# Kernel tuning notes

Hardware: AMD Instinct MI355X
Metric: run time of the kernel (lower is better)

Reference implementation:

```python
import jax, jax.numpy as jnp
import numpy as np

B, L, D = 2, 2048, 2048
NUM_HEADS = 32
KV_GROUPS = 8
GROUP_SIZE = NUM_HEADS // KV_GROUPS  # 4
HEAD_DIM = D // NUM_HEADS            # 64


def _rope_tables(L, hd):
    # standard RoPE angle tables, duplicated across halves to width hd
    inv_freq = 1.0 / (10000.0 ** (np.arange(0, hd, 2, dtype=np.float32) / hd))
    ang = np.arange(L, dtype=np.float32)[:, None] * inv_freq[None, :]  # [L, hd/2]
    cos = np.concatenate([np.cos(ang), np.cos(ang)], axis=-1)
    sin = np.concatenate([np.sin(ang), np.sin(ang)], axis=-1)
    return jnp.asarray(cos), jnp.asarray(sin)


def setup_inputs() -> dict:
    key = jax.random.key(0)
    ks = jax.random.split(key, 6)
    x = jax.random.normal(ks[0], (B, L, D), dtype=jnp.float32)
    mask = jnp.triu(jnp.ones((L, L), dtype=bool), k=1)  # causal: True above diag
    cos, sin = _rope_tables(L, HEAD_DIM)
    s = 0.02
    Wq = jax.random.normal(ks[1], (D, D), dtype=jnp.float32) * s
    Wk = jax.random.normal(ks[2], (D, KV_GROUPS * HEAD_DIM), dtype=jnp.float32) * s
    Wv = jax.random.normal(ks[3], (D, KV_GROUPS * HEAD_DIM), dtype=jnp.float32) * s
    Wo = jax.random.normal(ks[4], (D, D), dtype=jnp.float32) * s
    bo = jnp.zeros((D,), dtype=jnp.float32)
    return {"x": x, "mask": mask, "cos": cos, "sin": sin,
            "Wq": Wq, "Wk": Wk, "Wv": Wv, "Wo": Wo, "bo": bo}


def _apply_rope(t, cos, sin):
    # t: [B, H, L, hd]
    hd = t.shape[-1]
    t1, t2 = t[..., : hd // 2], t[..., hd // 2:]
    rotated = jnp.concatenate([-t2, t1], axis=-1)
    return t * cos[None, None, :, :] + rotated * sin[None, None, :, :]


def reference(x, mask, cos, sin, Wq, Wk, Wv, Wo, bo):
    Bv, Lv, Dv = x.shape
    hd = HEAD_DIM
    q = (x @ Wq).reshape(Bv, Lv, NUM_HEADS, hd).transpose(0, 2, 1, 3)   # [B,H,L,hd]
    k = (x @ Wk).reshape(Bv, Lv, KV_GROUPS, hd).transpose(0, 2, 1, 3)   # [B,G,L,hd]
    v = (x @ Wv).reshape(Bv, Lv, KV_GROUPS, hd).transpose(0, 2, 1, 3)
    q = _apply_rope(q, cos, sin)
    k = _apply_rope(k, cos, sin)
    k = jnp.repeat(k, GROUP_SIZE, axis=1)  # [B,H,L,hd]
    v = jnp.repeat(v, GROUP_SIZE, axis=1)
    scores = jnp.einsum('bhqd,bhkd->bhqk', q, k) / jnp.sqrt(jnp.float32(hd))
    scores = jnp.where(mask[None, None, :, :], -jnp.inf, scores)
    attn = jax.nn.softmax(scores, axis=-1)
    out = jnp.einsum('bhqk,bhkd->bhqd', attn, v)         # [B,H,L,hd]
    out = out.transpose(0, 2, 1, 3).reshape(Bv, Lv, Dv)  # [B,L,D]
    return out @ Wo + bo
```

## Files before the change

### kernel.cpp

```cpp
#include <hip/hip_runtime.h>
#include <cstdint>

typedef unsigned short UST;
typedef __bf16 v8bf __attribute__((ext_vector_type(8)));
typedef float v4f __attribute__((ext_vector_type(4)));

static __device__ __forceinline__ UST f2b(float f) {
  union { float f; uint32_t u; } c; c.f = f;
  uint32_t u = c.u;
  u += 0x7fffu + ((u >> 16) & 1u);
  return (UST)(u >> 16);
}
static __device__ __forceinline__ float b2f(UST h) {
  union { uint32_t u; float f; } c; c.u = ((uint32_t)h) << 16;
  return c.f;
}
static __device__ __forceinline__ uint32_t cvtpk(float lo, float hi) {
  uint32_t r;
  asm("v_cvt_pk_bf16_f32 %0, %1, %2" : "=v"(r) : "v"(lo), "v"(hi));
  return r;
}
static __device__ __forceinline__ float fexp2(float x) {
  float r;
  asm("v_exp_f32 %0, %1" : "=v"(r) : "v"(x));
  return r;
}

static __device__ __forceinline__ void gl_lds16(const UST* g, UST* l) {
  __builtin_amdgcn_global_load_lds(
      (const __attribute__((address_space(1))) void*)g,
      (__attribute__((address_space(3))) void*)l, 16, 0, 0);
}

__global__ __launch_bounds__(256) void k_cast(const float* __restrict__ src,
                                              UST* __restrict__ dst) {
  size_t i = (size_t)blockIdx.x * 256 + threadIdx.x;
  const float4* s4 = reinterpret_cast<const float4*>(src) + 2 * i;
  float4 a = s4[0], b = s4[1];
  union { UST s[8]; uint4 v; } r;
  r.s[0] = f2b(a.x); r.s[1] = f2b(a.y); r.s[2] = f2b(a.z); r.s[3] = f2b(a.w);
  r.s[4] = f2b(b.x); r.s[5] = f2b(b.y); r.s[6] = f2b(b.z); r.s[7] = f2b(b.w);
  reinterpret_cast<uint4*>(dst)[i] = r.v;
}

__global__ __launch_bounds__(256) void k_castT(const float* __restrict__ W,
                                               UST* __restrict__ dst, int N, int K) {
  __shared__ float tile[32][33];
  int nt = blockIdx.x * 32, kt = blockIdx.y * 32;
  int tx = threadIdx.x, ty = threadIdx.y;
#pragma unroll
  for (int r = 0; r < 4; ++r)
    tile[ty + r * 8][tx] = W[(size_t)(kt + ty + r * 8) * N + nt + tx];
  __syncthreads();
#pragma unroll
  for (int r = 0; r < 4; ++r)
    dst[(size_t)(nt + ty + r * 8) * K + kt + tx] = f2b(tile[tx][ty + r * 8]);
}

template <int EPI>
__global__ __launch_bounds__(256) void k_gemm(const UST* __restrict__ A,
                                              const UST* __restrict__ Bt,
                                              void* __restrict__ Cv,
                                              const float* __restrict__ bias,
                                              int M, int N, int K) {
  __shared__ __align__(16) UST a_s[128 * 32];
  __shared__ __align__(16) UST b_s[128 * 32];
  int tid = threadIdx.x;
  int lane = tid & 63, w = tid >> 6;
  int lr = lane & 15, lg = lane >> 4;
  int wr = w >> 1, wc = w & 1;
  int mBlk = blockIdx.y * 128, nBlk = blockIdx.x * 128;

  v4f acc[4][4];
#pragma unroll
  for (int i = 0; i < 4; ++i)
#pragma unroll
    for (int j = 0; j < 4; ++j) acc[i][j] = (v4f){0.f, 0.f, 0.f, 0.f};

  int stR = tid >> 2, stC = (tid & 3) * 8;
  const UST* Ag = A + (size_t)(mBlk + stR) * K + stC;
  const UST* Bg = Bt + (size_t)(nBlk + stR) * K + stC;
  UST* aL = a_s + w * 512;
  UST* bL = b_s + w * 512;
  size_t radv = (size_t)64 * K;

  for (int k0 = 0; k0 < K; k0 += 32) {
    __syncthreads();
    gl_lds16(Ag, aL);
    gl_lds16(Ag + radv, aL + 2048);
    gl_lds16(Bg, bL);
    gl_lds16(Bg + radv, bL + 2048);
    Ag += 32; Bg += 32;
    __syncthreads();
    v8bf af[4], bfv[4];
#pragma unroll
    for (int mt = 0; mt < 4; ++mt)
      af[mt] = *(const v8bf*)&a_s[(wr * 64 + mt * 16 + lr) * 32 + lg * 8];
#pragma unroll
    for (int nt = 0; nt < 4; ++nt)
      bfv[nt] = *(const v8bf*)&b_s[(wc * 64 + nt * 16 + lr) * 32 + lg * 8];
#pragma unroll
    for (int mt = 0; mt < 4; ++mt)
#pragma unroll
      for (int nt = 0; nt < 4; ++nt)
        acc[mt][nt] = __builtin_amdgcn_mfma_f32_16x16x32_bf16(af[mt], bfv[nt],
                                                              acc[mt][nt], 0, 0, 0);
  }

  int row0 = mBlk + wr * 64 + lg * 4;
  int col0 = nBlk + wc * 64 + lr;
#pragma unroll
  for (int mt = 0; mt < 4; ++mt)
#pragma unroll
    for (int nt = 0; nt < 4; ++nt)
#pragma unroll
      for (int r = 0; r < 4; ++r) {
        int row = row0 + mt * 16 + r;
        int col = col0 + nt * 16;
        if constexpr (EPI == 0) {
          ((UST*)Cv)[(size_t)row * N + col] = f2b(acc[mt][nt][r]);
        } else {
          ((float*)Cv)[(size_t)row * N + col] = acc[mt][nt][r] + bias[col];
        }
      }
}

__global__ __launch_bounds__(256) void k_rope(const UST* __restrict__ qkv,
                                              const float* __restrict__ cosT,
                                              const float* __restrict__ sinT,
                                              UST* __restrict__ qh,
                                              UST* __restrict__ kh) {
  int idx = blockIdx.x * 256 + threadIdx.x;
  int d = idx & 31;
  int hh = (idx >> 5) % 40;
  int row = idx / 1280;
  int l = row & 2047, b = row >> 11;
  int col = (hh < 32) ? hh * 64 : 2048 + (hh - 32) * 64;
  float t1 = b2f(qkv[(size_t)row * 3072 + col + d]);
  float t2 = b2f(qkv[(size_t)row * 3072 + col + d + 32]);
  float c = cosT[l * 64 + d], s = sinT[l * 64 + d];
  float o1 = t1 * c - t2 * s;
  float o2 = t2 * c + t1 * s;
  if (hh < 32) {
    size_t base = (((size_t)b * 32 + hh) * 2048 + l) * 64 + d;
    qh[base] = f2b(o1 * 0.125f);
    qh[base + 32] = f2b(o2 * 0.125f);
  } else {
    size_t base = (((size_t)b * 8 + (hh - 32)) * 2048 + l) * 64 + d;
    kh[base] = f2b(o1);
    kh[base + 32] = f2b(o2);
  }
}

__global__ __launch_bounds__(256) void k_vtrans(const UST* __restrict__ qkv,
                                                UST* __restrict__ vt) {
  __shared__ __align__(16) UST tl[64][72];
  int lt = blockIdx.x, bg = blockIdx.y;
  int b = bg >> 3, g = bg & 7;
  int t = threadIdx.x;
  int li = t >> 2, d0 = (t & 3) * 16;
  const UST* src = qkv + (size_t)(b * 2048 + lt * 64 + li) * 3072 + 2560 + g * 64 + d0;
  *(uint4*)&tl[li][d0] = *(const uint4*)src;
  *(uint4*)&tl[li][d0 + 8] = *(const uint4*)(src + 8);
  __syncthreads();
  int d = t >> 2, l0 = (t & 3) * 16;
  union { UST u[8]; uint4 v; } r0, r1;
#pragma unroll
  for (int e = 0; e < 8; ++e) r0.u[e] = tl[l0 + e][d];
#pragma unroll
  for (int e = 0; e < 8; ++e) r1.u[e] = tl[l0 + 8 + e][d];
  UST* dstp = vt + (size_t)((b * 8 + g) * 64 + d) * 2048 + (size_t)lt * 64 + l0;
  *(uint4*)dstp = r0.v;
  *(uint4*)(dstp + 8) = r1.v;
}

__global__ __launch_bounds__(512, 4) void k_attn(const UST* __restrict__ qh,
                                                 const UST* __restrict__ kh,
                                                 const UST* __restrict__ vt,
                                                 UST* __restrict__ outp) {
  __shared__ __align__(16) UST k_s[128 * 72];
  __shared__ __align__(16) UST v_s[64 * 136];
  __shared__ __align__(16) UST p_s[8][16 * 136];
  int bx = blockIdx.x, h = blockIdx.y, b = blockIdx.z;
  int g = h >> 2;
  int tid = threadIdx.x, w = tid >> 6, lane = tid & 63;
  int lr = lane & 15, lg = lane >> 4;

  int ksr = tid >> 2, ksc = (tid & 3) * 16;
  int vsr = tid >> 3, vsc = (tid & 7) * 16;
  const UST* kbase = kh + ((size_t)(b * 8 + g) * 2048 + ksr) * 64 + ksc;
  const UST* vbase = vt + ((size_t)(b * 8 + g) * 64 + vsr) * 2048 + vsc;
  UST* kdst = &k_s[ksr * 72 + ksc];
  UST* vdst = &v_s[vsr * 136 + vsc];

  for (int half = 0; half < 2; ++half) {
    int qt = half ? (15 - bx) : bx;
    int qbase = qt * 128 + w * 16;

    const UST* qp = qh + ((size_t)(b * 32 + h) * 2048 + qbase + lr) * 64 + lg * 8;
    v8bf qf0 = *(const v8bf*)qp;
    v8bf qf1 = *(const v8bf*)(qp + 32);

    float m = -1e30f, ls = 0.f;
    v4f o[4];
#pragma unroll
    for (int dt = 0; dt < 4; ++dt) o[dt] = (v4f){0.f, 0.f, 0.f, 0.f};

    __syncthreads();
    uint4 pk0 = *(const uint4*)kbase, pk1 = *(const uint4*)(kbase + 8);
    uint4 pv0 = *(const uint4*)vbase, pv1 = *(const uint4*)(vbase + 8);
    *(uint4*)kdst = pk0; *(uint4*)(kdst + 8) = pk1;
    *(uint4*)vdst = pv0; *(uint4*)(vdst + 8) = pv1;

    for (int j = 0; j <= qt; ++j) {
      __syncthreads();
      bool pref = (j < qt);
      if (pref) {
        const UST* kg = kbase + (size_t)(j + 1) * 8192;
        const UST* vg = vbase + (j + 1) * 128;
        pk0 = *(const uint4*)kg; pk1 = *(const uint4*)(kg + 8);
        pv0 = *(const uint4*)vg; pv1 = *(const uint4*)(vg + 8);
      }

      v4f st[8];
#pragma unroll
      for (int kt = 0; kt < 8; ++kt) {
        const UST* kr = &k_s[(kt * 16 + lr) * 72 + lg * 8];
        v8bf kf0 = *(const v8bf*)kr;
        v8bf kf1 = *(const v8bf*)(kr + 32);
        v4f z = (v4f){0.f, 0.f, 0.f, 0.f};
        z = __builtin_amdgcn_mfma_f32_16x16x32_bf16(kf0, qf0, z, 0, 0, 0);
        z = __builtin_amdgcn_mfma_f32_16x16x32_bf16(kf1, qf1, z, 0, 0, 0);
        st[kt] = z;
      }
      if (j == qt) {
        int qg = qbase + lr;
#pragma unroll
        for (int kt = 0; kt < 8; ++kt)
#pragma unroll
          for (int r = 0; r < 4; ++r) {
            int kg2 = j * 128 + kt * 16 + 4 * lg + r;
            if (kg2 > qg) st[kt][r] = -1e30f;
          }
      }

      float t0 = fmaxf(fmaxf(st[0][0], st[0][1]), fmaxf(st[0][2], st[0][3]));
      float t1 = fmaxf(fmaxf(st[1][0], st[1][1]), fmaxf(st[1][2], st[1][3]));
      float t2 = fmaxf(fmaxf(st[2][0], st[2][1]), fmaxf(st[2][2], st[2][3]));
      float t3 = fmaxf(fmaxf(st[3][0], st[3][1]), fmaxf(st[3][2], st[3][3]));
      float t4 = fmaxf(fmaxf(st[4][0], st[4][1]), fmaxf(st[4][2], st[4][3]));
      float t5 = fmaxf(fmaxf(st[5][0], st[5][1]), fmaxf(st[5][2], st[5][3]));
      float t6 = fmaxf(fmaxf(st[6][0], st[6][1]), fmaxf(st[6][2], st[6][3]));
      float t7 = fmaxf(fmaxf(st[7][0], st[7][1]), fmaxf(st[7][2], st[7][3]));
      float mx = fmaxf(fmaxf(fmaxf(t0, t1), fmaxf(t2, t3)),
                       fmaxf(fmaxf(t4, t5), fmaxf(t6, t7)));
      mx = fmaxf(mx, __shfl_xor(mx, 16));
      mx = fmaxf(mx, __shfl_xor(mx, 32));

      if (!__all(mx <= m + 8.f)) {
        float mn = fmaxf(m, mx);
        float al = __expf(m - mn);
        m = mn;
        ls *= al;
#pragma unroll
        for (int r = 0; r < 4; ++r) {
          float ar = __shfl(al, 4 * lg + r);
          o[0][r] *= ar; o[1][r] *= ar; o[2][r] *= ar; o[3][r] *= ar;
        }
      }

      constexpr float LOG2E = 1.44269504f;
      float mlog = m * LOG2E;
      float rs = 0.f;
      UST* pw = &p_s[w][lr * 136 + 4 * lg];
#pragma unroll
      for (int kt = 0; kt < 8; ++kt) {
        float p0 = fexp2(__builtin_fmaf(st[kt][0], LOG2E, -mlog));
        float p1 = fexp2(__builtin_fmaf(st[kt][1], LOG2E, -mlog));
        float p2 = fexp2(__builtin_fmaf(st[kt][2], LOG2E, -mlog));
        float p3 = fexp2(__builtin_fmaf(st[kt][3], LOG2E, -mlog));
        rs += (p0 + p1) + (p2 + p3);
        uint2 q2;
        q2.x = cvtpk(p0, p1);
        q2.y = cvtpk(p2, p3);
        *(uint2*)(pw + kt * 16) = q2;
      }
      rs += __shfl_xor(rs, 16);
      rs += __shfl_xor(rs, 32);
      ls += rs;

#pragma unroll
      for (int kk = 0; kk < 4; ++kk) {
        v8bf pa = *(const v8bf*)&p_s[w][lr * 136 + kk * 32 + lg * 8];
#pragma unroll
        for (int dt = 0; dt < 4; ++dt) {
          v8bf vb = *(const v8bf*)&v_s[(dt * 16 + lr) * 136 + kk * 32 + lg * 8];
          o[dt] = __builtin_amdgcn_mfma_f32_16x16x32_bf16(pa, vb, o[dt], 0, 0, 0);
        }
      }

      __syncthreads();
      if (pref) {
        *(uint4*)kdst = pk0; *(uint4*)(kdst + 8) = pk1;
        *(uint4*)vdst = pv0; *(uint4*)(vdst + 8) = pv1;
      }
    }

    float iv = 1.f / ls;
#pragma unroll
    for (int r = 0; r < 4; ++r) {
      float ivr = __shfl(iv, 4 * lg + r);
      size_t rowb = ((size_t)b * 2048 + qbase + 4 * lg + r) * 2048 + h * 64 + lr;
#pragma unroll
      for (int dt = 0; dt < 4; ++dt)
        outp[rowb + dt * 16] = f2b(o[dt][r] * ivr);
    }
  }
}

extern "C" void kernel_launch(void* const* d_in, const int* in_sizes, int n_in,
                              void* d_out, int out_size, void* d_ws, size_t ws_size,
                              hipStream_t stream) {
  const float* x    = (const float*)d_in[0];
  const float* cosT = (const float*)d_in[2];
  const float* sinT = (const float*)d_in[3];
  const float* Wq   = (const float*)d_in[4];
  const float* Wk   = (const float*)d_in[5];
  const float* Wv   = (const float*)d_in[6];
  const float* Wo   = (const float*)d_in[7];
  const float* bo   = (const float*)d_in[8];
  float* out = (float*)d_out;

  char* ws = (char*)d_ws;
  UST* xb   = (UST*)(ws);
  UST* wcat = (UST*)(ws + 16777216);
  UST* wot  = (UST*)(ws + 29360128);
  UST* qkv  = (UST*)(ws + 37748736);
  UST* qhp  = (UST*)(ws + 62914560);
  UST* khp  = (UST*)(ws + 79691776);
  UST* vtp  = (UST*)(ws + 83886080);
  UST* attn_o = xb;

  k_cast<<<4096, 256, 0, stream>>>(x, xb);
  k_castT<<<dim3(64, 64), dim3(32, 8), 0, stream>>>(Wq, wcat, 2048, 2048);
  k_castT<<<dim3(16, 64), dim3(32, 8), 0, stream>>>(Wk, wcat + (size_t)2048 * 2048, 512, 2048);
  k_castT<<<dim3(16, 64), dim3(32, 8), 0, stream>>>(Wv, wcat + (size_t)2560 * 2048, 512, 2048);
  k_castT<<<dim3(64, 64), dim3(32, 8), 0, stream>>>(Wo, wot, 2048, 2048);

  k_gemm<0><<<dim3(24, 32), 256, 0, stream>>>(xb, wcat, qkv, nullptr, 4096, 3072, 2048);
  k_rope<<<20480, 256, 0, stream>>>(qkv, cosT, sinT, qhp, khp);
  k_vtrans<<<dim3(32, 16), 256, 0, stream>>>(qkv, vtp);
  k_attn<<<dim3(8, 32, 2), 512, 0, stream>>>(qhp, khp, vtp, attn_o);
  k_gemm<1><<<dim3(16, 32), 256, 0, stream>>>(attn_o, wot, out, bo, 4096, 2048, 2048);
}
```

Before: 227.7 us.

## Replace GEMM with larger-tile double-buffered pipelined kernel and add MFMA priority hints

Replaces the simple 128x128 single-buffered GEMM with a templated 256-wide tile kernel using 512 threads. It double-buffers the async global-to-LDS loads with explicit vmcnt waits and interleaves staging with MFMA halves. It also adds a grid swizzle for L2 locality and raises wave priority around MFMA sections in both the GEMM and the attention kernel. This aims to hide global load latency and raise MFMA utilisation, at the cost of more LDS per block and hand-tuned waitcnt logic that is fragile.

```diff
diff --git a/kernel.cpp b/kernel.cpp
--- a/kernel.cpp
+++ b/kernel.cpp
@@ -24,6 +24,10 @@
   float r;
   asm("v_exp_f32 %0, %1" : "=v"(r) : "v"(x));
   return r;
+}
+template <int N>
+static __device__ __forceinline__ void wait_vm() {
+  asm volatile("s_waitcnt vmcnt(%0)" :: "i"(N));
 }
 
 static __device__ __forceinline__ void gl_lds16(const UST* g, UST* l) {
@@ -57,70 +61,122 @@
     dst[(size_t)(nt + ty + r * 8) * K + kt + tx] = f2b(tile[tx][ty + r * 8]);
 }
 
-template <int EPI>
-__global__ __launch_bounds__(256) void k_gemm(const UST* __restrict__ A,
-                                              const UST* __restrict__ Bt,
-                                              void* __restrict__ Cv,
-                                              const float* __restrict__ bias,
-                                              int M, int N, int K) {
-  __shared__ __align__(16) UST a_s[128 * 32];
-  __shared__ __align__(16) UST b_s[128 * 32];
-  int tid = threadIdx.x;
-  int lane = tid & 63, w = tid >> 6;
+template <int BM, int BN, int WM, int WN, int EPI>
+__global__ __launch_bounds__(512, 2) void k_gemm2(const UST* __restrict__ A,
+                                                  const UST* __restrict__ Bt,
+                                                  void* __restrict__ Cv,
+                                                  const float* __restrict__ bias,
+                                                  int M, int N, int K, int ntn) {
+  constexpr int WMR = BM / WM, WNR = BN / WN;
+  constexpr int MF = WMR / 16, NF = WNR / 16, MH = MF / 2;
+  constexpr int CA = BM / 128, CB = BN / 128;
+  constexpr int NKEEP = 2 * CA + CB;
+  constexpr int AELEMS = 4 * BM * 32;
+  __shared__ __align__(16) UST lds[AELEMS + 4 * BN * 32];
+
+  int tid = threadIdx.x, w = tid >> 6, lane = tid & 63;
   int lr = lane & 15, lg = lane >> 4;
-  int wr = w >> 1, wc = w & 1;
-  int mBlk = blockIdx.y * 128, nBlk = blockIdx.x * 128;
-
-  v4f acc[4][4];
-#pragma unroll
-  for (int i = 0; i < 4; ++i)
-#pragma unroll
-    for (int j = 0; j < 4; ++j) acc[i][j] = (v4f){0.f, 0.f, 0.f, 0.f};
-
-  int stR = tid >> 2, stC = (tid & 3) * 8;
-  const UST* Ag = A + (size_t)(mBlk + stR) * K + stC;
-  const UST* Bg = Bt + (size_t)(nBlk + stR) * K + stC;
-  UST* aL = a_s + w * 512;
-  UST* bL = b_s + w * 512;
-  size_t radv = (size_t)64 * K;
-
-  for (int k0 = 0; k0 < K; k0 += 32) {
-    __syncthreads();
-    gl_lds16(Ag, aL);
-    gl_lds16(Ag + radv, aL + 2048);
-    gl_lds16(Bg, bL);
-    gl_lds16(Bg + radv, bL + 2048);
-    Ag += 32; Bg += 32;
-    __syncthreads();
-    v8bf af[4], bfv[4];
-#pragma unroll
-    for (int mt = 0; mt < 4; ++mt)
-      af[mt] = *(const v8bf*)&a_s[(wr * 64 + mt * 16 + lr) * 32 + lg * 8];
-#pragma unroll
-    for (int nt = 0; nt < 4; ++nt)
-      bfv[nt] = *(const v8bf*)&b_s[(wc * 64 + nt * 16 + lr) * 32 + lg * 8];
-#pragma unroll
-    for (int mt = 0; mt < 4; ++mt)
-#pragma unroll
-      for (int nt = 0; nt < 4; ++nt)
-        acc[mt][nt] = __builtin_amdgcn_mfma_f32_16x16x32_bf16(af[mt], bfv[nt],
-                                                              acc[mt][nt], 0, 0, 0);
+  int wm = w / WN, wn = w % WN;
+
+  int T = (int)gridDim.x;
+  int q = T >> 3;
+  int bid = (int)blockIdx.x;
+  int swz = (bid & 7) * q + (bid >> 3);
+  int mBlk = (swz / ntn) * BM, nBlk = (swz % ntn) * BN;
+
+  v4f acc[MF][NF];
+#pragma unroll
+  for (int i = 0; i < MF; ++i)
+#pragma unroll
+    for (int j = 0; j < NF; ++j) acc[i][j] = (v4f){0.f, 0.f, 0.f, 0.f};
+
+  int srow = tid >> 2, scol = (tid & 3) * 8;
+  const UST* Abase = A + (size_t)(mBlk + srow) * K + scol;
+  const UST* Bbase = Bt + (size_t)(nBlk + srow) * K + scol;
+  int ldsW = w * 512;
+
+  auto stageA = [&](int buf, int s, int kt) {
+#pragma unroll
+    for (int i = 0; i < CA; ++i)
+      gl_lds16(Abase + (size_t)(i * 128) * K + kt * 64 + s * 32,
+               &lds[(buf * 2 + s) * BM * 32 + i * 4096 + ldsW]);
+  };
+  auto stageB = [&](int buf, int s, int kt) {
+#pragma unroll
+    for (int i = 0; i < CB; ++i)
+      gl_lds16(Bbase + (size_t)(i * 128) * K + kt * 64 + s * 32,
+               &lds[AELEMS + (buf * 2 + s) * BN * 32 + i * 4096 + ldsW]);
+  };
+  auto ldA = [&](int buf, int s, int mh, int f) -> v8bf {
+    int row = wm * WMR + mh * (WMR / 2) + f * 16 + lr;
+    return *(const v8bf*)&lds[((buf * 2 + s) * BM + row) * 32 + lg * 8];
+  };
+  auto ldB = [&](int buf, int s, int nf) -> v8bf {
+    int row = wn * WNR + nf * 16 + lr;
+    return *(const v8bf*)&lds[AELEMS + ((buf * 2 + s) * BN + row) * 32 + lg * 8];
+  };
+
+  int NT = K >> 6;
+  stageA(0, 0, 0); stageB(0, 0, 0); stageA(0, 1, 0); stageB(0, 1, 0);
+
+  for (int kt = 0; kt < NT; ++kt) {
+    int buf = kt & 1, nb = buf ^ 1;
+    bool more = (kt + 1 < NT);
+#pragma unroll
+    for (int s = 0; s < 2; ++s) {
+      if (more) {
+        stageA(nb, s, kt + 1);
+        wait_vm<NKEEP>();
+      } else {
+        if (s == 0) wait_vm<CA + CB>(); else wait_vm<0>();
+      }
+      __builtin_amdgcn_s_barrier();
+      __builtin_amdgcn_sched_barrier(0);
+      v8bf bfr[NF], afr[MH];
+#pragma unroll
+      for (int nf = 0; nf < NF; ++nf) bfr[nf] = ldB(buf, s, nf);
+#pragma unroll
+      for (int f = 0; f < MH; ++f) afr[f] = ldA(buf, s, 0, f);
+      __builtin_amdgcn_s_setprio(1);
+#pragma unroll
+      for (int f = 0; f < MH; ++f)
+#pragma unroll
+        for (int nf = 0; nf < NF; ++nf)
+          acc[f][nf] = __builtin_amdgcn_mfma_f32_16x16x32_bf16(afr[f], bfr[nf],
+                                                               acc[f][nf], 0, 0, 0);
+      __builtin_amdgcn_s_setprio(0);
+      __builtin_amdgcn_s_barrier();
+      if (more) stageB(nb, s, kt + 1);
+      __builtin_amdgcn_s_barrier();
+      __builtin_amdgcn_sched_barrier(0);
+#pragma unroll
+      for (int f = 0; f < MH; ++f) afr[f] = ldA(buf, s, 1, f);
+      __builtin_amdgcn_s_setprio(1);
+#pragma unroll
+      for (int f = 0; f < MH; ++f)
+#pragma unroll
+        for (int nf = 0; nf < NF; ++nf)
+          acc[MH + f][nf] = __builtin_amdgcn_mfma_f32_16x16x32_bf16(afr[f], bfr[nf],
+                                                                    acc[MH + f][nf], 0, 0, 0);
+      __builtin_amdgcn_s_setprio(0);
+      __builtin_amdgcn_s_barrier();
+    }
   }
 
-  int row0 = mBlk + wr * 64 + lg * 4;
-  int col0 = nBlk + wc * 64 + lr;
-#pragma unroll
-  for (int mt = 0; mt < 4; ++mt)
-#pragma unroll
-    for (int nt = 0; nt < 4; ++nt)
+  int row0 = mBlk + wm * WMR + lg * 4;
+  int col0 = nBlk + wn * WNR + lr;
+#pragma unroll
+  for (int fm = 0; fm < MF; ++fm)
+#pragma unroll
+    for (int nf = 0; nf < NF; ++nf)
 #pragma unroll
       for (int r = 0; r < 4; ++r) {
-        int row = row0 + mt * 16 + r;
-        int col = col0 + nt * 16;
+        int row = row0 + fm * 16 + r;
+        int col = col0 + nf * 16;
         if constexpr (EPI == 0) {
-          ((UST*)Cv)[(size_t)row * N + col] = f2b(acc[mt][nt][r]);
+          ((UST*)Cv)[(size_t)row * N + col] = f2b(acc[fm][nf][r]);
         } else {
-          ((float*)Cv)[(size_t)row * N + col] = acc[mt][nt][r] + bias[col];
+          ((float*)Cv)[(size_t)row * N + col] = acc[fm][nf][r] + bias[col];
         }
       }
 }
@@ -223,6 +279,7 @@
       }
 
       v4f st[8];
+      __builtin_amdgcn_s_setprio(1);
 #pragma unroll
       for (int kt = 0; kt < 8; ++kt) {
         const UST* kr = &k_s[(kt * 16 + lr) * 72 + lg * 8];
@@ -233,6 +290,7 @@
         z = __builtin_amdgcn_mfma_f32_16x16x32_bf16(kf1, qf1, z, 0, 0, 0);
         st[kt] = z;
       }
+      __builtin_amdgcn_s_setprio(0);
       if (j == qt) {
         int qg = qbase + lr;
 #pragma unroll
@@ -289,6 +347,7 @@
       rs += __shfl_xor(rs, 32);
       ls += rs;
 
+      __builtin_amdgcn_s_setprio(1);
 #pragma unroll
       for (int kk = 0; kk < 4; ++kk) {
         v8bf pa = *(const v8bf*)&p_s[w][lr * 136 + kk * 32 + lg * 8];
@@ -298,6 +357,7 @@
           o[dt] = __builtin_amdgcn_mfma_f32_16x16x32_bf16(pa, vb, o[dt], 0, 0, 0);
         }
       }
+      __builtin_amdgcn_s_setprio(0);
 
       __syncthreads();
       if (pref) {
@@ -347,9 +407,11 @@
   k_castT<<<dim3(16, 64), dim3(32, 8), 0, stream>>>(Wv, wcat + (size_t)2560 * 2048, 512, 2048);
   k_castT<<<dim3(64, 64), dim3(32, 8), 0, stream>>>(Wo, wot, 2048, 2048);
 
-  k_gemm<0><<<dim3(24, 32), 256, 0, stream>>>(xb, wcat, qkv, nullptr, 4096, 3072, 2048);
+  k_gemm2<256, 256, 2, 4, 0><<<192, 512, 0, stream>>>(xb, wcat, qkv, nullptr,
+                                                      4096, 3072, 2048, 12);
   k_rope<<<20480, 256, 0, stream>>>(qkv, cosT, sinT, qhp, khp);
   k_vtrans<<<dim3(32, 16), 256, 0, stream>>>(qkv, vtp);
   k_attn<<<dim3(8, 32, 2), 512, 0, stream>>>(qhp, khp, vtp, attn_o);
-  k_gemm<1><<<dim3(16, 32), 256, 0, stream>>>(attn_o, wot, out, bo, 4096, 2048, 2048);
-}
+  k_gemm2<256, 128, 4, 2, 1><<<256, 512, 0, stream>>>(attn_o, wot, out, bo,
+                                                      4096, 2048, 2048, 16);
+}
```

Measured after the change: 219.6 us. 1.04x faster.
